# Optimization experiments

Hardware: AMD Instinct MI355X
Metric: run time of the kernel (lower is better)

The kernel has to match this reference:

```python
import jax, jax.numpy as jnp
import numpy as np

TOP_K = 2
N_EXP = 64
EVAL_CAPACITY = 2.0


def setup_inputs() -> dict:
    key = jax.random.key(0)
    k1, k2 = jax.random.split(key)
    x = jax.random.normal(k1, (4, 4096, 2048), dtype=jnp.float32)
    w_g = jax.random.normal(k2, (N_EXP, 2048), dtype=jnp.float32) * 0.02  # Linear(n_embd, n_exp, bias=False)
    return {"x": x, "w_g": w_g}


def reference(x, w_g):
    B, T, C = x.shape
    num_tokens = B * T
    x_flat = x.reshape(num_tokens, C)
    # gating logits: [N, E]
    logits = jnp.einsum('nc,ec->ne', x_flat, w_g)
    # top-k selection
    top_k_logits, top_k_indices = jax.lax.top_k(logits, TOP_K)  # [N, k]
    router_probs = jax.nn.softmax(top_k_logits, axis=-1)        # [N, k]
    # static expert capacity (eval path)
    exp_capacity = max(int(TOP_K * EVAL_CAPACITY * num_tokens / N_EXP), 4)
    # one-hot expert mask [N, k, E]
    expert_mask = jax.nn.one_hot(top_k_indices, N_EXP, dtype=jnp.int32)
    # rank tokens within each expert via cumsum over (k-major, token) order
    reshaped = expert_mask.transpose(1, 0, 2).reshape(TOP_K * num_tokens, N_EXP)
    cumsum = jnp.cumsum(reshaped, axis=0)
    position = cumsum.reshape(TOP_K, num_tokens, N_EXP).transpose(1, 0, 2)  # [N, k, E]
    rank = (position - 1) * expert_mask
    capacity_mask = (rank < exp_capacity).astype(jnp.int32)
    final_mask = expert_mask * capacity_mask                     # [N, k, E]
    probs_mask = (final_mask.sum(axis=-1) > 0)                   # [N, k] bool
    router_probs_masked = router_probs * probs_mask.astype(router_probs.dtype)
    final_rank = rank.sum(axis=-1)                               # [N, k]
    return final_mask, router_probs_masked, top_k_indices, final_rank, exp_capacity
```

## Files before the change

### kernel.cpp

```cpp
#include <hip/hip_runtime.h>
#include <math.h>

#define C_DIM 2048
#define E_DIM 64
#define BT    32
#define NW    4

typedef _Float16 v8hf  __attribute__((ext_vector_type(8)));
typedef float    f32x4 __attribute__((ext_vector_type(4)));

#define SCALE      64.0f
#define INV_SCALE2 (1.0f/4096.0f)

__launch_bounds__(256)
__global__ void k_wsplit(const float* __restrict__ w, _Float16* __restrict__ wfrag)
{
    int t  = blockIdx.x * 256 + threadIdx.x;
    int l  = t & 63;
    int ni = (t >> 6) & 3;
    int q  = t >> 8;
    int e  = 16 * ni + (l & 15);
    int k0 = 32 * q + (l >> 4) * 8;
    const float* src = w + (size_t)e * C_DIM + k0;
    float4 a = *(const float4*)(src);
    float4 b = *(const float4*)(src + 4);
    float s[8] = {a.x, a.y, a.z, a.w, b.x, b.y, b.z, b.w};
    v8hf hv, lv;
#pragma unroll
    for (int j = 0; j < 8; ++j) {
        float sc = s[j] * SCALE;
        _Float16 h = (_Float16)sc;
        hv[j] = h;
        lv[j] = (_Float16)(sc - (float)h);
    }
    size_t fo = (size_t)(q * 4 + ni) * 1024;
    *(v8hf*)(wfrag + fo + l * 8)       = hv;
    *(v8hf*)(wfrag + fo + 512 + l * 8) = lv;
}

__launch_bounds__(256)
__global__ void k_logits_top2(const float* __restrict__ x, const _Float16* __restrict__ wfrag,
                              unsigned char* __restrict__ idx0, unsigned char* __restrict__ idx1,
                              float* __restrict__ dlt, unsigned short* __restrict__ gcounts,
                              int nblk)
{
    __shared__ float lgs[BT * E_DIM];
    __shared__ int   cnt[128];

    const int tid  = threadIdx.x;
    const int lane = tid & 63;
    const int wk   = tid >> 6;
    const int ln15 = lane & 15;
    const int g    = lane >> 4;
    const int t0   = blockIdx.x * BT;

    if (tid < 128) cnt[tid] = 0;

    f32x4 acc[2][4];
#pragma unroll
    for (int mi = 0; mi < 2; ++mi)
#pragma unroll
        for (int ni = 0; ni < 4; ++ni) acc[mi][ni] = (f32x4)0.0f;

    const float* xb = x + (size_t)(t0 + ln15) * C_DIM + 32 * wk + 8 * g;
    const char*  wb = (const char*)wfrag + ((size_t)wk << 13) + (lane << 4);

    float4 axf[2][2][2];
    v8hf   bhf[2][4], blf[2][4];

#define LOADSTEP(c, s)                                                          \
    {                                                                           \
        _Pragma("unroll")                                                       \
        for (int mi = 0; mi < 2; ++mi) {                                        \
            const float* p = xb + (size_t)(16 * mi) * C_DIM + (c) * 128;        \
            axf[s][mi][0] = *(const float4*)(p);                                \
            axf[s][mi][1] = *(const float4*)(p + 4);                            \
        }                                                                       \
        const char* wp = wb + (size_t)(c) * 32768;                              \
        _Pragma("unroll")                                                       \
        for (int ni = 0; ni < 4; ++ni) {                                        \
            bhf[s][ni] = *(const v8hf*)(wp + ni * 2048);                        \
            blf[s][ni] = *(const v8hf*)(wp + ni * 2048 + 1024);                 \
        }                                                                       \
    }

#define DOSTEP(s)                                                               \
    {                                                                           \
        v8hf ah[2], al[2];                                                      \
        _Pragma("unroll")                                                       \
        for (int mi = 0; mi < 2; ++mi) {                                        \
            float sv[8] = {axf[s][mi][0].x, axf[s][mi][0].y, axf[s][mi][0].z,   \
                           axf[s][mi][0].w, axf[s][mi][1].x, axf[s][mi][1].y,   \
                           axf[s][mi][1].z, axf[s][mi][1].w};                   \
            _Pragma("unroll")                                                   \
            for (int j = 0; j < 8; ++j) {                                       \
                float sc = sv[j] * SCALE;                                       \
                _Float16 h = (_Float16)sc;                                      \
                ah[mi][j] = h;                                                  \
                al[mi][j] = (_Float16)(sc - (float)h);                          \
            }                                                                   \
        }                                                                       \
        _Pragma("unroll")                                                       \
        for (int ni = 0; ni < 4; ++ni)                                          \
            _Pragma("unroll")                                                   \
            for (int mi = 0; mi < 2; ++mi) {                                    \
                acc[mi][ni] = __builtin_amdgcn_mfma_f32_16x16x32_f16(ah[mi], bhf[s][ni], acc[mi][ni], 0, 0, 0); \
                acc[mi][ni] = __builtin_amdgcn_mfma_f32_16x16x32_f16(ah[mi], blf[s][ni], acc[mi][ni], 0, 0, 0); \
                acc[mi][ni] = __builtin_amdgcn_mfma_f32_16x16x32_f16(al[mi], bhf[s][ni], acc[mi][ni], 0, 0, 0); \
            }                                                                   \
    }

    LOADSTEP(0, 0);
#pragma unroll
    for (int c = 0; c < 16; ++c) {
        const int cur = c & 1;
        if (c < 15) LOADSTEP(c + 1, cur ^ 1);
        DOSTEP(cur);
    }

#pragma unroll
    for (int w = 0; w < NW; ++w) {
        if (w > 0) __syncthreads();
        if (wk == w) {
#pragma unroll
            for (int mi = 0; mi < 2; ++mi)
#pragma unroll
                for (int ni = 0; ni < 4; ++ni)
#pragma unroll
                    for (int gg = 0; gg < 4; ++gg) {
                        int row = 16 * mi + (g << 2) + gg;
                        int e   = 16 * ni + ln15;
                        float vv = acc[mi][ni][gg] * INV_SCALE2;
                        if (w == 0) lgs[row * 64 + e]  = vv;
                        else        lgs[row * 64 + e] += vv;
                    }
        }
    }
    __syncthreads();

#pragma unroll
    for (int t = 0; t < 8; ++t) {
        int rowl = (wk << 3) + t;
        float v = lgs[rowl * 64 + lane];
        float vv = v; int ix = lane;
#pragma unroll
        for (int off = 32; off > 0; off >>= 1) {
            float ov = __shfl_down(vv, off, 64);
            int   oi = __shfl_down(ix, off, 64);
            if (ov > vv || (ov == vv && oi < ix)) { vv = ov; ix = oi; }
        }
        int   i1 = __shfl(ix, 0, 64);
        float v1 = __shfl(vv, 0, 64);

        vv = (lane == i1) ? -3.0e38f : v; ix = lane;
#pragma unroll
        for (int off = 32; off > 0; off >>= 1) {
            float ov = __shfl_down(vv, off, 64);
            int   oi = __shfl_down(ix, off, 64);
            if (ov > vv || (ov == vv && oi < ix)) { vv = ov; ix = oi; }
        }
        int   i2 = __shfl(ix, 0, 64);
        float v2 = __shfl(vv, 0, 64);

        if (lane == 0) {
            int n = t0 + rowl;
            idx0[n] = (unsigned char)i1;
            idx1[n] = (unsigned char)i2;
            dlt[n]  = v2 - v1;
            atomicAdd(&cnt[i1], 1);
            atomicAdd(&cnt[64 + i2], 1);
        }
    }

    __syncthreads();
    if (tid < 128) {
        int e = tid & 63, k = tid >> 6;
        gcounts[(size_t)e * (2 * nblk) + k * nblk + blockIdx.x] = (unsigned short)cnt[tid];
    }
}

__launch_bounds__(64)
__global__ void k_scan2(unsigned short* __restrict__ g, int S)
{
    const int e = blockIdx.x, lane = threadIdx.x;
    unsigned short* row = g + (size_t)e * S;
    int vals[16];
    const int R = S >> 6;
#pragma unroll
    for (int r = 0; r < 16; ++r) if (r < R) vals[r] = row[(r << 6) + lane];
    int running = 0;
#pragma unroll
    for (int r = 0; r < 16; ++r) {
        if (r >= R) break;
        int v = vals[r], s = v;
#pragma unroll
        for (int off = 1; off < 64; off <<= 1) {
            int t = __shfl_up(s, off, 64);
            if (lane >= off) s += t;
        }
        row[(r << 6) + lane] = (unsigned short)(s - v + running);
        running += __shfl(s, 63, 64);
    }
}

__launch_bounds__(128)
__global__ void k_rank_out(const unsigned char* __restrict__ idx0, const unsigned char* __restrict__ idx1,
                           const unsigned short* __restrict__ gpre, const float* __restrict__ dlt,
                           float* __restrict__ out, int N, int cap, int nblk)
{
    const int b = blockIdx.x, tid = threadIdx.x;
    const int lane = tid & 63, kk = tid >> 6;
    const int t0 = b * BT;
    __shared__ int sm_ix[2][BT], sm_rk[2][BT];

    int v = -1, base = 0;
    if (lane < BT) {
        v = (kk ? idx1 : idx0)[t0 + lane];
        base = gpre[(size_t)v * (2 * nblk) + kk * nblk + b];
    }
    const unsigned long long ltm = (1ull << lane) - 1ull;
    int pre = 0;
    for (int e = 0; e < 64; ++e) {
        unsigned long long bb = __ballot(v == e);
        if (v == e) pre = __popcll(bb & ltm);
    }
    if (lane < BT) { sm_ix[kk][lane] = v; sm_rk[kk][lane] = base + pre; }
    __syncthreads();

#pragma unroll
    for (int rep = 0; rep < 8; ++rep) {
        int f   = tid + 128 * rep;
        int n2  = f >> 5;
        int rem = (f & 31) * 4;
        int kq  = rem >> 6;
        int e0  = rem & 63;
        int ix  = sm_ix[kq][n2];
        int rr  = sm_rk[kq][n2];
        float val = (rr < cap) ? 1.0f : 0.0f;
        float4 o = make_float4(0.f, 0.f, 0.f, 0.f);
        int d = ix - e0;
        if (d >= 0 && d < 4) ((float*)&o)[d] = val;
        *(float4*)(out + (size_t)(t0 + n2) * 128 + rem) = o;
    }

    size_t B = (size_t)2 * N * E_DIM;
    if (tid < 2 * BT) {
        int n2 = tid >> 1, kq = tid & 1;
        int n  = t0 + n2;
        int gi = 2 * n + kq;
        int ix = sm_ix[kq][n2];
        int rr = sm_rk[kq][n2];
        float d  = dlt[n];
        float e1 = expf(d);
        float inv = 1.0f / (1.0f + e1);
        float p  = kq ? (e1 * inv) : inv;
        bool keep = rr < cap;
        out[B + gi]         = keep ? p : 0.0f;
        out[B + 2 * N + gi] = (float)ix;
        out[B + 4 * N + gi] = (float)rr;
    }
    if (b == 0 && tid == 0) out[B + 6 * N] = (float)cap;
}

extern "C" void kernel_launch(void* const* d_in, const int* in_sizes, int n_in,
                              void* d_out, int out_size, void* d_ws, size_t ws_size,
                              hipStream_t stream)
{
    const float* x  = (const float*)d_in[0];
    const float* wg = (const float*)d_in[1];
    const int N = in_sizes[0] / C_DIM;
    const int nblk = N / BT;

    char* ws = (char*)d_ws;
    unsigned char*  idx0    = (unsigned char*)ws;
    unsigned char*  idx1    = idx0 + N;
    float*          dlt     = (float*)(idx1 + N);
    unsigned short* gcounts = (unsigned short*)(dlt + N);
    _Float16*       wfrag   = (_Float16*)(gcounts + (size_t)64 * 2 * nblk);

    float* out = (float*)d_out;

    int cap = (int)((long long)2 * 2 * N / E_DIM);
    if (cap < 4) cap = 4;

    k_wsplit<<<64, 256, 0, stream>>>(wg, wfrag);
    k_logits_top2<<<nblk, 256, 0, stream>>>(x, wfrag, idx0, idx1, dlt, gcounts, nblk);
    k_scan2<<<E_DIM, 64, 0, stream>>>(gcounts, 2 * nblk);
    k_rank_out<<<nblk, 128, 0, stream>>>(idx0, idx1, gcounts, dlt, out, N, cap, nblk);
}
```

Baseline: 253.7 us.

## Stream x tiles into LDS via async global_load_lds with a 4-deep pipeline

Replaces the register double-buffered x loads with direct global-to-LDS loads (global_load_lds) into a 4-stage ring buffer, issued three chunks ahead, with manual vmcnt waits. W fragments stay in registers but are double-buffered. This aims to keep more memory requests in flight and cut register pressure so the streaming GEMM is closer to bandwidth-bound. The risks are the 64KB LDS allocation, which limits occupancy, and the hand-counted vmcnt, which relies on the compiler not reordering or adding other memory operations.

```diff
diff --git a/kernel.cpp b/kernel.cpp
--- a/kernel.cpp
+++ b/kernel.cpp
@@ -11,6 +11,14 @@
 
 #define SCALE      64.0f
 #define INV_SCALE2 (1.0f/4096.0f)
+
+typedef __attribute__((address_space(3))) char lds_char;
+
+__device__ __forceinline__ void gl16(const void* g, lds_char* l)
+{
+    __builtin_amdgcn_global_load_lds((const __attribute__((address_space(1))) void*)g,
+                                     (__attribute__((address_space(3))) void*)l, 16, 0, 0);
+}
 
 __launch_bounds__(256)
 __global__ void k_wsplit(const float* __restrict__ w, _Float16* __restrict__ wfrag)
@@ -44,80 +52,101 @@
                               float* __restrict__ dlt, unsigned short* __restrict__ gcounts,
                               int nblk)
 {
-    __shared__ float lgs[BT * E_DIM];
-    __shared__ int   cnt[128];
+    __shared__ alignas(16) char smem[65536];
 
     const int tid  = threadIdx.x;
     const int lane = tid & 63;
     const int wk   = tid >> 6;
     const int ln15 = lane & 15;
-    const int g    = lane >> 4;
+    const int g4   = lane >> 4;
     const int t0   = blockIdx.x * BT;
 
-    if (tid < 128) cnt[tid] = 0;
-
     f32x4 acc[2][4];
 #pragma unroll
     for (int mi = 0; mi < 2; ++mi)
 #pragma unroll
         for (int ni = 0; ni < 4; ++ni) acc[mi][ni] = (f32x4)0.0f;
 
-    const float* xb = x + (size_t)(t0 + ln15) * C_DIM + 32 * wk + 8 * g;
-    const char*  wb = (const char*)wfrag + ((size_t)wk << 13) + (lane << 4);
-
-    float4 axf[2][2][2];
-    v8hf   bhf[2][4], blf[2][4];
-
-#define LOADSTEP(c, s)                                                          \
-    {                                                                           \
+    v8hf bh[2][4], bl[2][4];
+    v8hf ah[2], al[2];
+
+    const float* xlane = x + (size_t)(t0 + ln15) * C_DIM + 32 * wk + 8 * g4;
+    const char*  wlane = (const char*)wfrag + (lane << 4);
+    lds_char* s3    = (lds_char*)smem;
+    lds_char* sbase = s3 + wk * 4096;
+
+#define ISSUE_X(cc)                                                             \
+    do {                                                                        \
+        lds_char*    d  = sbase + (((cc) & 3) * 16384);                         \
+        const float* gp = xlane + (cc) * 128;                                   \
+        gl16(gp,                  d);                                           \
+        gl16(gp + 4,              d + 1024);                                    \
+        gl16(gp + 16 * C_DIM,     d + 2048);                                    \
+        gl16(gp + 16 * C_DIM + 4, d + 3072);                                    \
+    } while (0)
+
+#define ISSUE_B(cc, s)                                                          \
+    do {                                                                        \
+        const char* wp = wlane + ((size_t)(4 * (cc) + wk) << 13);               \
+        bh[s][0] = *(const v8hf*)(wp);          bl[s][0] = *(const v8hf*)(wp + 1024); \
+        bh[s][1] = *(const v8hf*)(wp + 2048);   bl[s][1] = *(const v8hf*)(wp + 3072); \
+        bh[s][2] = *(const v8hf*)(wp + 4096);   bl[s][2] = *(const v8hf*)(wp + 5120); \
+        bh[s][3] = *(const v8hf*)(wp + 6144);   bl[s][3] = *(const v8hf*)(wp + 7168); \
+    } while (0)
+
+#define CVT(mi, lo, hi)                                                         \
+    do {                                                                        \
         _Pragma("unroll")                                                       \
-        for (int mi = 0; mi < 2; ++mi) {                                        \
-            const float* p = xb + (size_t)(16 * mi) * C_DIM + (c) * 128;        \
-            axf[s][mi][0] = *(const float4*)(p);                                \
-            axf[s][mi][1] = *(const float4*)(p + 4);                            \
+        for (int j = 0; j < 4; ++j) {                                           \
+            float sc0 = (lo)[j] * SCALE;                                        \
+            _Float16 h0 = (_Float16)sc0;                                        \
+            ah[mi][j] = h0; al[mi][j] = (_Float16)(sc0 - (float)h0);            \
+            float sc1 = (hi)[j] * SCALE;                                        \
+            _Float16 h1 = (_Float16)sc1;                                        \
+            ah[mi][j + 4] = h1; al[mi][j + 4] = (_Float16)(sc1 - (float)h1);    \
         }                                                                       \
-        const char* wp = wb + (size_t)(c) * 32768;                              \
+    } while (0)
+
+#define COMPUTE(cc, s)                                                          \
+    do {                                                                        \
+        const char* rb = smem + wk * 4096 + (((cc) & 3) * 16384) + lane * 16;   \
+        f32x4 lo0 = *(const f32x4*)(rb);                                        \
+        f32x4 hi0 = *(const f32x4*)(rb + 1024);                                 \
+        f32x4 lo1 = *(const f32x4*)(rb + 2048);                                 \
+        f32x4 hi1 = *(const f32x4*)(rb + 3072);                                 \
+        CVT(0, lo0, hi0);                                                       \
+        CVT(1, lo1, hi1);                                                       \
         _Pragma("unroll")                                                       \
         for (int ni = 0; ni < 4; ++ni) {                                        \
-            bhf[s][ni] = *(const v8hf*)(wp + ni * 2048);                        \
-            blf[s][ni] = *(const v8hf*)(wp + ni * 2048 + 1024);                 \
+            acc[0][ni] = __builtin_amdgcn_mfma_f32_16x16x32_f16(ah[0], bh[s][ni], acc[0][ni], 0, 0, 0); \
+            acc[0][ni] = __builtin_amdgcn_mfma_f32_16x16x32_f16(ah[0], bl[s][ni], acc[0][ni], 0, 0, 0); \
+            acc[0][ni] = __builtin_amdgcn_mfma_f32_16x16x32_f16(al[0], bh[s][ni], acc[0][ni], 0, 0, 0); \
+            acc[1][ni] = __builtin_amdgcn_mfma_f32_16x16x32_f16(ah[1], bh[s][ni], acc[1][ni], 0, 0, 0); \
+            acc[1][ni] = __builtin_amdgcn_mfma_f32_16x16x32_f16(ah[1], bl[s][ni], acc[1][ni], 0, 0, 0); \
+            acc[1][ni] = __builtin_amdgcn_mfma_f32_16x16x32_f16(al[1], bh[s][ni], acc[1][ni], 0, 0, 0); \
         }                                                                       \
-    }
-
-#define DOSTEP(s)                                                               \
-    {                                                                           \
-        v8hf ah[2], al[2];                                                      \
-        _Pragma("unroll")                                                       \
-        for (int mi = 0; mi < 2; ++mi) {                                        \
-            float sv[8] = {axf[s][mi][0].x, axf[s][mi][0].y, axf[s][mi][0].z,   \
-                           axf[s][mi][0].w, axf[s][mi][1].x, axf[s][mi][1].y,   \
-                           axf[s][mi][1].z, axf[s][mi][1].w};                   \
-            _Pragma("unroll")                                                   \
-            for (int j = 0; j < 8; ++j) {                                       \
-                float sc = sv[j] * SCALE;                                       \
-                _Float16 h = (_Float16)sc;                                      \
-                ah[mi][j] = h;                                                  \
-                al[mi][j] = (_Float16)(sc - (float)h);                          \
-            }                                                                   \
-        }                                                                       \
-        _Pragma("unroll")                                                       \
-        for (int ni = 0; ni < 4; ++ni)                                          \
-            _Pragma("unroll")                                                   \
-            for (int mi = 0; mi < 2; ++mi) {                                    \
-                acc[mi][ni] = __builtin_amdgcn_mfma_f32_16x16x32_f16(ah[mi], bhf[s][ni], acc[mi][ni], 0, 0, 0); \
-                acc[mi][ni] = __builtin_amdgcn_mfma_f32_16x16x32_f16(ah[mi], blf[s][ni], acc[mi][ni], 0, 0, 0); \
-                acc[mi][ni] = __builtin_amdgcn_mfma_f32_16x16x32_f16(al[mi], bhf[s][ni], acc[mi][ni], 0, 0, 0); \
-            }                                                                   \
-    }
-
-    LOADSTEP(0, 0);
-#pragma unroll
-    for (int c = 0; c < 16; ++c) {
-        const int cur = c & 1;
-        if (c < 15) LOADSTEP(c + 1, cur ^ 1);
-        DOSTEP(cur);
-    }
-
+    } while (0)
+
+#define CHUNK(c, CUR, NXT)                                                      \
+    ISSUE_X(((c) + 3) & 15);                                                    \
+    ISSUE_B(((c) + 1) & 15, NXT);                                               \
+    asm volatile("s_waitcnt vmcnt(28)" ::: "memory");                           \
+    COMPUTE(c, CUR);
+
+    ISSUE_X(0); ISSUE_X(1); ISSUE_X(2);
+    ISSUE_B(0, 0);
+
+    CHUNK(0, 0, 1)  CHUNK(1, 1, 0)  CHUNK(2, 0, 1)  CHUNK(3, 1, 0)
+    CHUNK(4, 0, 1)  CHUNK(5, 1, 0)  CHUNK(6, 0, 1)  CHUNK(7, 1, 0)
+    CHUNK(8, 0, 1)  CHUNK(9, 1, 0)  CHUNK(10, 0, 1) CHUNK(11, 1, 0)
+    CHUNK(12, 0, 1) CHUNK(13, 1, 0) CHUNK(14, 0, 1) CHUNK(15, 1, 0)
+
+    asm volatile("s_waitcnt vmcnt(0)" ::: "memory");
+    __syncthreads();
+
+    float* lgs = (float*)smem;
+    int*   cnt = (int*)(smem + 8192);
+    if (tid < 128) cnt[tid] = 0;
 #pragma unroll
     for (int w = 0; w < NW; ++w) {
         if (w > 0) __syncthreads();
@@ -128,7 +157,7 @@
                 for (int ni = 0; ni < 4; ++ni)
 #pragma unroll
                     for (int gg = 0; gg < 4; ++gg) {
-                        int row = 16 * mi + (g << 2) + gg;
+                        int row = 16 * mi + (g4 << 2) + gg;
                         int e   = 16 * ni + ln15;
                         float vv = acc[mi][ni][gg] * INV_SCALE2;
                         if (w == 0) lgs[row * 64 + e]  = vv;
```

Measured after the change: 237.7 us. 6.3% less time.
